# Kernel optimization log

Measured on AMD Instinct MI355X. Metric: run time of the kernel, lower is better.

The kernel has to match this reference:

```python
import jax, jax.numpy as jnp
import numpy as np

DT = 0.01          # discretization timestep (init kwarg dt)
DAMP_MIN = 5e-4    # minimum damping (init kwarg damp_min)
BATCH, SEQ, D_IN, N_STATE = 16, 2048, 1024, 128


def setup_inputs() -> dict:
    key = jax.random.key(0)
    k1, k2, k3, k4, k5 = jax.random.split(key, 5)
    u = jax.random.normal(k1, (BATCH, SEQ, D_IN), jnp.float32)
    # A_real init: randn*0.1 - damp_min, then clamped to <= -damp_min (stability)
    A_real = jnp.minimum(jax.random.normal(k2, (N_STATE,), jnp.float32) * 0.1 - DAMP_MIN, -DAMP_MIN)
    A_imag = jax.random.normal(k3, (N_STATE,), jnp.float32)
    B = jax.random.normal(k4, (N_STATE, D_IN), jnp.float32) * 0.02
    C = jax.random.normal(k5, (D_IN, N_STATE), jnp.float32) * 0.02
    return {"u": u, "A_real": A_real, "A_imag": A_imag, "B": B, "C": C}


def reference(u, A_real, A_imag, B, C):
    """Real-input path of StableResonantSSM.

    Bilinear discretization of diagonal complex A:
      a_disc = (1 + dt/2 * a) / (1 - dt/2 * a)          (elementwise, A diagonal)
      B_disc = sqrt(dt) * B / (1 - dt/2 * a)            (row-wise scaling)
    Recurrence: h_t = a_disc * h_{t-1} + B_disc @ u_t;  y_t = Re(C @ h_t).
    """
    dt = jnp.float32(DT)
    a = (A_real + 1j * A_imag).astype(jnp.complex64)          # (N,)
    denom = 1.0 - (dt / 2) * a                                 # (N,) complex
    a_disc = (1.0 + (dt / 2) * a) / denom                      # (N,)
    B_disc = (jnp.sqrt(dt) * B.astype(jnp.complex64)) / denom[:, None]  # (N, D)

    # Precompute all input injections as one GEMM: (T, B, N) complex
    Bu = jnp.einsum('btd,nd->tbn', u, B_disc)

    def step(h, bu_t):
        h = a_disc * h + bu_t
        return h, h

    h0 = jnp.zeros((u.shape[0], a.shape[0]), jnp.complex64)
    _, hs = jax.lax.scan(step, h0, Bu)                         # hs: (T, B, N)

    # C is real, so Re(C @ h) == C @ Re(h)
    y = jnp.einsum('tbn,dn->btd', hs.real, C)                  # (B, T, D)
    return y
```

## Files before the change

### kernel.cpp

```cpp
#include <hip/hip_runtime.h>
#include <hip/hip_bf16.h>
#include <cstdint>

#define DT_F    0.01f
#define NB      16
#define T_SEQ   2048
#define DD      1024
#define NS      128
#define CHUNK   64
#define NCH     32

using f32x4  = __attribute__((ext_vector_type(4))) float;
using bf16x8 = __attribute__((ext_vector_type(8))) short;
using fl4    = __attribute__((ext_vector_type(4))) float;

#define AS1(p) ((const __attribute__((address_space(1))) void*)(p))
#define AS3(p) ((__attribute__((address_space(3))) void*)(p))

__device__ __forceinline__ unsigned short f2bf(float f) {
  union { float f; unsigned u; } v; v.f = f;
  unsigned r = v.u + 0x7fffu + ((v.u >> 16) & 1u);
  return (unsigned short)(r >> 16);
}
__device__ __forceinline__ float bf2f(unsigned short s) {
  union { unsigned u; float f; } v; v.u = ((unsigned)s) << 16;
  return v.f;
}
__device__ __forceinline__ unsigned short f2bf_hw(float f) {
  __hip_bfloat16 h = __float2bfloat16(f);
  return __builtin_bit_cast(unsigned short, h);
}

__device__ __forceinline__ void adisc_full(float Arn, float Ain,
                                           float& ar, float& ai,
                                           float& cr, float& ci) {
  const float dr = 1.f - 0.5f * DT_F * Arn;
  const float di = -0.5f * DT_F * Ain;
  const float inv = 1.f / (dr * dr + di * di);
  const float nr = 1.f + 0.5f * DT_F * Arn;
  const float nim = 0.5f * DT_F * Ain;
  ar = (nr * dr + nim * di) * inv;
  ai = (nim * dr - nr * di) * inv;
  const float s = sqrtf(DT_F);
  cr = s * dr * inv;
  ci = -s * di * inv;
}
__device__ __forceinline__ void adisc(float Arn, float Ain, float& ar, float& ai) {
  float cr, ci; adisc_full(Arn, Ain, ar, ai, cr, ci);
}

__global__ void prep_all(const float* __restrict__ B, const float* __restrict__ C,
                         unsigned short* __restrict__ Bb, unsigned short* __restrict__ Cb) {
  const int blk = blockIdx.x;
  const int tid = threadIdx.x;
  if (blk < 512) {
    const int i = blk * 256 + tid;
    Cb[i] = f2bf(C[i]);
  } else {
    const int i = (blk - 512) * 256 + tid;
    Bb[i] = f2bf(B[i]);
  }
}

__global__ __launch_bounds__(512, 4) void gemm1s(const float* __restrict__ U,
                                                 const float* __restrict__ Ar,
                                                 const float* __restrict__ Ai,
                                                 const unsigned short* __restrict__ Bb,
                                                 unsigned short* __restrict__ Hs,
                                                 float* __restrict__ F) {
  __shared__ __align__(16) char smem[24576];
  char* As = smem;
  char* Bs = smem + 8192;
  char* Bt = smem;

  const int tid  = threadIdx.x;
  const int lane = tid & 63;
  const int wave = tid >> 6;
  const int blk  = blockIdx.x;
  const size_t m0 = (size_t)blk * CHUNK;

  f32x4 acc[4];
  const f32x4 zero = {0.f, 0.f, 0.f, 0.f};
#pragma unroll
  for (int i = 0; i < 4; ++i) acc[i] = zero;

  const int srow = tid >> 3;
  const int scol = (tid & 7) * 8;
  const int sb   = srow * 128 + (((tid & 7) * 16) ^ ((srow & 7) << 4));
  const int growl = lane >> 3;
  const int gcolsw = 8 * ((lane & 7) ^ (lane >> 3));

  for (int k0 = 0; k0 < DD; k0 += 64) {
    __syncthreads();
#pragma unroll
    for (int g = 0; g < 2; ++g) {
      const int row = wave * 16 + g * 8;
      const unsigned short* gb = Bb + (size_t)(row + growl) * DD + k0 + gcolsw;
      __builtin_amdgcn_global_load_lds(AS1(gb), AS3(Bs + row * 128), 16, 0, 0);
    }
    {
      const float* ga = U + (m0 + srow) * DD + k0 + scol;
      fl4 v0 = *(const fl4*)ga;
      fl4 v1 = *(const fl4*)(ga + 4);
      bf16x8 p0;
#pragma unroll
      for (int e = 0; e < 4; ++e) {
        p0[e] = (short)f2bf_hw(v0[e]); p0[4 + e] = (short)f2bf_hw(v1[e]);
      }
      *(bf16x8*)(As + sb) = p0;
    }
    __syncthreads();
#pragma unroll
    for (int ks = 0; ks < 2; ++ks) {
      const int colb = ks * 64 + (lane >> 4) * 16;
      bf16x8 af[4], bfr;
#pragma unroll
      for (int i = 0; i < 4; ++i) {
        const int r = i * 16 + (lane & 15);
        af[i] = *(const bf16x8*)(As + r * 128 + (colb ^ ((r & 7) << 4)));
      }
      {
        const int r = wave * 16 + (lane & 15);
        bfr = *(const bf16x8*)(Bs + r * 128 + (colb ^ ((r & 7) << 4)));
      }
#pragma unroll
      for (int i = 0; i < 4; ++i)
        acc[i] = __builtin_amdgcn_mfma_f32_16x16x32_bf16(af[i], bfr, acc[i], 0, 0, 0);
    }
  }
  __syncthreads();

#pragma unroll
  for (int i = 0; i < 4; ++i) {
    const int n = wave * 16 + (lane & 15);
#pragma unroll
    for (int q = 0; q < 4; ++q) {
      const int t = i * 16 + (lane >> 4) * 4 + q;
      *(unsigned short*)(Bt + t * 256 + ((n * 2) ^ ((t & 7) << 4))) = f2bf_hw(acc[i][q]);
    }
  }
  __syncthreads();

  if (tid < 128) {
    const int n = tid;
    float ar, ai, cr, ci; adisc_full(Ar[n], Ai[n], ar, ai, cr, ci);
    float hr = 0.f, hi = 0.f;
    unsigned short* o = Hs + (size_t)blk * (CHUNK * NS) + n;
#pragma unroll 8
    for (int t = 0; t < CHUNK; ++t) {
      const float s = bf2f(*(const unsigned short*)(Bt + t * 256 + ((n * 2) ^ ((t & 7) << 4))));
      const float br = cr * s;
      const float bi = ci * s;
      const float xr = fmaf(ar, hr, fmaf(-ai, hi, br));
      const float xi = fmaf(ar, hi, fmaf(ai, hr, bi));
      hr = xr; hi = xi;
      o[t * NS] = f2bf(hr);
    }
    F[(size_t)blk * 256 + n]       = hr;
    F[(size_t)blk * 256 + 128 + n] = hi;
  }
}

__global__ void carry_scan(const float* __restrict__ F,
                           const float* __restrict__ Ar, const float* __restrict__ Ai,
                           float* __restrict__ G) {
  __shared__ float Fl[NCH * 256];
  const int b = blockIdx.x;
  const int tid = threadIdx.x;
  const float4* src = (const float4*)(F + (size_t)b * NCH * 256);
  float4* dst = (float4*)Fl;
#pragma unroll
  for (int i = 0; i < NCH * 64 / 256; ++i)
    dst[tid + i * 256] = src[tid + i * 256];
  __syncthreads();
  if (tid < 128) {
    const int n = tid;
    float ar, ai; adisc(Ar[n], Ai[n], ar, ai);
    float alr = ar, ali = ai;
#pragma unroll
    for (int s = 0; s < 6; ++s) {
      const float tr = alr * alr - ali * ali;
      const float ti = 2.f * alr * ali;
      alr = tr; ali = ti;
    }
    float cr = 0.f, ci = 0.f;
    for (int c = 0; c < NCH; ++c) {
      const size_t idx = ((size_t)b * NCH + c) * 256 + n;
      G[idx]       = ar * cr - ai * ci;
      G[idx + 128] = ar * ci + ai * cr;
      const float fr = Fl[c * 256 + n];
      const float fi = Fl[c * 256 + 128 + n];
      const float xr = fmaf(alr, cr, fmaf(-ali, ci, fr));
      const float xi = fmaf(alr, ci, fmaf(ali, cr, fi));
      cr = xr; ci = xi;
    }
  }
}

__global__ __launch_bounds__(512, 4) void gemm2s(const unsigned short* __restrict__ Hs,
                                                 const float* __restrict__ G,
                                                 const float* __restrict__ Ar,
                                                 const float* __restrict__ Ai,
                                                 const unsigned short* __restrict__ Cb,
                                                 float* __restrict__ y) {
  __shared__ __align__(16) char Hl[64 * 256];
  const int tid  = threadIdx.x;
  const int lane = tid & 63;
  const int wave = tid >> 6;
  const int blk  = blockIdx.x;
  const int c    = blk & 31;
  const size_t m0 = (size_t)blk * CHUNK;

  const char* tile = (const char*)Hs + (size_t)blk * (CHUNK * NS * 2);
#pragma unroll
  for (int g = 0; g < 2; ++g) {
    const int r0 = wave * 8 + g * 4;
    const int r  = r0 + (lane >> 4);
    const int srcOff = r * 256 + ((((lane & 15)) * 16) ^ ((r & 7) << 4));
    __builtin_amdgcn_global_load_lds(AS1(tile + srcOff), AS3(Hl + r0 * 256), 16, 0, 0);
  }
  __syncthreads();

  if (c != 0 && tid < 128) {
    const int n = tid;
    float ar, ai; adisc(Ar[n], Ai[n], ar, ai);
    float gr = G[(size_t)blk * 256 + n];
    float gi = G[(size_t)blk * 256 + 128 + n];
#pragma unroll 8
    for (int t = 0; t < CHUNK; ++t) {
      unsigned short* pp = (unsigned short*)(Hl + t * 256 + ((n * 2) ^ ((t & 7) << 4)));
      *pp = f2bf(bf2f(*pp) + gr);
      const float xr = ar * gr - ai * gi;
      const float xi = ar * gi + ai * gr;
      gr = xr; gi = xi;
    }
  }
  __syncthreads();

  const f32x4 zero = {0.f, 0.f, 0.f, 0.f};
#pragma unroll
  for (int cg = 0; cg < 4; ++cg) {
    const int d0 = (cg * 8 + wave) * 32;
    f32x4 oacc[4][2];
#pragma unroll
    for (int i = 0; i < 4; ++i)
#pragma unroll
      for (int j = 0; j < 2; ++j) oacc[i][j] = zero;

#pragma unroll
    for (int ks = 0; ks < 4; ++ks) {
      bf16x8 af[4], bfr[2];
#pragma unroll
      for (int i = 0; i < 4; ++i) {
        const int r = i * 16 + (lane & 15);
        af[i] = *(const bf16x8*)(Hl + r * 256 + ((ks * 64 + (lane >> 4) * 16) ^ ((r & 7) << 4)));
      }
#pragma unroll
      for (int j = 0; j < 2; ++j)
        bfr[j] = *(const bf16x8*)(Cb + (size_t)(d0 + j * 16 + (lane & 15)) * NS + ks * 32 + (lane >> 4) * 8);
#pragma unroll
      for (int i = 0; i < 4; ++i)
#pragma unroll
        for (int j = 0; j < 2; ++j)
          oacc[i][j] = __builtin_amdgcn_mfma_f32_16x16x32_bf16(af[i], bfr[j], oacc[i][j], 0, 0, 0);
    }
#pragma unroll
    for (int i = 0; i < 4; ++i) {
      const size_t r0 = m0 + i * 16 + (lane >> 4) * 4;
#pragma unroll
      for (int j = 0; j < 2; ++j) {
        const int d = d0 + j * 16 + (lane & 15);
#pragma unroll
        for (int q = 0; q < 4; ++q)
          y[(r0 + q) * DD + d] = oacc[i][j][q];
      }
    }
  }
}

extern "C" void kernel_launch(void* const* d_in, const int* in_sizes, int n_in,
                              void* d_out, int out_size, void* d_ws, size_t ws_size,
                              hipStream_t stream) {
  const float* u  = (const float*)d_in[0];
  const float* Ar = (const float*)d_in[1];
  const float* Ai = (const float*)d_in[2];
  const float* B  = (const float*)d_in[3];
  const float* C  = (const float*)d_in[4];
  float* y = (float*)d_out;
  char* ws = (char*)d_ws;

  unsigned short* Bb = (unsigned short*)(ws);
  unsigned short* Cb = (unsigned short*)(ws + (256 << 10));
  float*          F  = (float*)(ws + (512 << 10));
  float*          G  = (float*)(ws + (1024 << 10));
  unsigned short* Hs = (unsigned short*)(ws + (1536 << 10));

  prep_all<<<dim3(1024), dim3(256), 0, stream>>>(B, C, Bb, Cb);
  gemm1s<<<dim3(NB * NCH), dim3(512), 0, stream>>>(u, Ar, Ai, Bb, Hs, F);
  carry_scan<<<dim3(NB), dim3(256), 0, stream>>>(F, Ar, Ai, G);
  gemm2s<<<dim3(NB * NCH), dim3(512), 0, stream>>>(Hs, G, Ar, Ai, Cb, y);
}
```

Baseline: 72.64 us.

## Fold inter-chunk carry scan into second GEMM and use nontemporal streaming accesses

Removes the separate carry_scan kernel launch. Each gemm2s block now recomputes its own incoming carry by scanning the final states of all preceding chunks in its batch. This drops one launch and the G round trip through memory, at the cost of redundant serial work, up to 31 steps per block, done by 128 threads. It also marks the u loads in gemm1s and the y stores in gemm2s as nontemporal to reduce cache pollution from streaming data.

```diff
diff --git a/kernel.cpp b/kernel.cpp
--- a/kernel.cpp
+++ b/kernel.cpp
@@ -100,8 +100,8 @@
     }
     {
       const float* ga = U + (m0 + srow) * DD + k0 + scol;
-      fl4 v0 = *(const fl4*)ga;
-      fl4 v1 = *(const fl4*)(ga + 4);
+      fl4 v0 = __builtin_nontemporal_load((const fl4*)ga);
+      fl4 v1 = __builtin_nontemporal_load((const fl4*)(ga + 4));
       bf16x8 p0;
 #pragma unroll
       for (int e = 0; e < 4; ++e) {
@@ -161,44 +161,8 @@
   }
 }
 
-__global__ void carry_scan(const float* __restrict__ F,
-                           const float* __restrict__ Ar, const float* __restrict__ Ai,
-                           float* __restrict__ G) {
-  __shared__ float Fl[NCH * 256];
-  const int b = blockIdx.x;
-  const int tid = threadIdx.x;
-  const float4* src = (const float4*)(F + (size_t)b * NCH * 256);
-  float4* dst = (float4*)Fl;
-#pragma unroll
-  for (int i = 0; i < NCH * 64 / 256; ++i)
-    dst[tid + i * 256] = src[tid + i * 256];
-  __syncthreads();
-  if (tid < 128) {
-    const int n = tid;
-    float ar, ai; adisc(Ar[n], Ai[n], ar, ai);
-    float alr = ar, ali = ai;
-#pragma unroll
-    for (int s = 0; s < 6; ++s) {
-      const float tr = alr * alr - ali * ali;
-      const float ti = 2.f * alr * ali;
-      alr = tr; ali = ti;
-    }
-    float cr = 0.f, ci = 0.f;
-    for (int c = 0; c < NCH; ++c) {
-      const size_t idx = ((size_t)b * NCH + c) * 256 + n;
-      G[idx]       = ar * cr - ai * ci;
-      G[idx + 128] = ar * ci + ai * cr;
-      const float fr = Fl[c * 256 + n];
-      const float fi = Fl[c * 256 + 128 + n];
-      const float xr = fmaf(alr, cr, fmaf(-ali, ci, fr));
-      const float xi = fmaf(alr, ci, fmaf(ali, cr, fi));
-      cr = xr; ci = xi;
-    }
-  }
-}
-
 __global__ __launch_bounds__(512, 4) void gemm2s(const unsigned short* __restrict__ Hs,
-                                                 const float* __restrict__ G,
+                                                 const float* __restrict__ F,
                                                  const float* __restrict__ Ar,
                                                  const float* __restrict__ Ai,
                                                  const unsigned short* __restrict__ Cb,
@@ -224,8 +188,24 @@
   if (c != 0 && tid < 128) {
     const int n = tid;
     float ar, ai; adisc(Ar[n], Ai[n], ar, ai);
-    float gr = G[(size_t)blk * 256 + n];
-    float gi = G[(size_t)blk * 256 + 128 + n];
+    float alr = ar, ali = ai;
+#pragma unroll
+    for (int s = 0; s < 6; ++s) {
+      const float tr = alr * alr - ali * ali;
+      const float ti = 2.f * alr * ali;
+      alr = tr; ali = ti;
+    }
+    float cr = 0.f, ci = 0.f;
+    const float* Fb = F + (size_t)(blk - c) * 256;
+    for (int cc = 0; cc < c; ++cc) {
+      const float fr = Fb[(size_t)cc * 256 + n];
+      const float fi = Fb[(size_t)cc * 256 + 128 + n];
+      const float xr = fmaf(alr, cr, fmaf(-ali, ci, fr));
+      const float xi = fmaf(alr, ci, fmaf(ali, cr, fi));
+      cr = xr; ci = xi;
+    }
+    float gr = ar * cr - ai * ci;
+    float gi = ar * ci + ai * cr;
 #pragma unroll 8
     for (int t = 0; t < CHUNK; ++t) {
       unsigned short* pp = (unsigned short*)(Hl + t * 256 + ((n * 2) ^ ((t & 7) << 4)));
@@ -272,7 +252,7 @@
         const int d = d0 + j * 16 + (lane & 15);
 #pragma unroll
         for (int q = 0; q < 4; ++q)
-          y[(r0 + q) * DD + d] = oacc[i][j][q];
+          __builtin_nontemporal_store(oacc[i][j][q], &y[(r0 + q) * DD + d]);
       }
     }
   }
@@ -292,11 +272,9 @@
   unsigned short* Bb = (unsigned short*)(ws);
   unsigned short* Cb = (unsigned short*)(ws + (256 << 10));
   float*          F  = (float*)(ws + (512 << 10));
-  float*          G  = (float*)(ws + (1024 << 10));
-  unsigned short* Hs = (unsigned short*)(ws + (1536 << 10));
+  unsigned short* Hs = (unsigned short*)(ws + (1024 << 10));
 
   prep_all<<<dim3(1024), dim3(256), 0, stream>>>(B, C, Bb, Cb);
   gemm1s<<<dim3(NB * NCH), dim3(512), 0, stream>>>(u, Ar, Ai, Bb, Hs, F);
-  carry_scan<<<dim3(NB), dim3(256), 0, stream>>>(F, Ar, Ai, G);
-  gemm2s<<<dim3(NB * NCH), dim3(512), 0, stream>>>(Hs, G, Ar, Ai, Cb, y);
-}
+  gemm2s<<<dim3(NB * NCH), dim3(512), 0, stream>>>(Hs, F, Ar, Ai, Cb, y);
+}
```

New measurement: 100.9 us. 1.39x slower.
